# Kernel optimization log

Hardware: AMD Instinct MI355X
Metric: run time of the kernel (lower is better)

The kernel has to match this reference:

```python
import jax, jax.numpy as jnp
import numpy as np

HEAD_SIZE = 128
LAMBDA_INIT = 0.8
FILL = 1e-09  # the module fills masked positions with 1e-9 (not -inf); reproduce faithfully


def setup_inputs() -> dict:
    key = jax.random.key(0)
    ks = jax.random.split(key, 12)
    B, T, C = 8, 2048, 1024
    q = jax.random.normal(ks[0], (B, T, C), dtype=jnp.float32)
    k = jax.random.normal(ks[1], (B, T, C), dtype=jnp.float32)
    v = jax.random.normal(ks[2], (B, T, C), dtype=jnp.float32)
    pad_mask = jax.random.randint(ks[3], (B, T), 0, 2, dtype=jnp.int32)
    scale = 1.0 / np.sqrt(C)
    Wq = jax.random.normal(ks[4], (C, 2 * HEAD_SIZE), dtype=jnp.float32) * scale
    Wk = jax.random.normal(ks[5], (C, 2 * HEAD_SIZE), dtype=jnp.float32) * scale
    Wv = jax.random.normal(ks[6], (C, HEAD_SIZE), dtype=jnp.float32) * scale
    lq1 = jax.random.normal(ks[7], (HEAD_SIZE,), dtype=jnp.float32)
    lk1 = jax.random.normal(ks[8], (HEAD_SIZE,), dtype=jnp.float32)
    lq2 = jax.random.normal(ks[9], (HEAD_SIZE,), dtype=jnp.float32)
    lk2 = jax.random.normal(ks[10], (HEAD_SIZE,), dtype=jnp.float32)
    return {"q": q, "k": k, "v": v, "pad_mask": pad_mask,
            "Wq": Wq, "Wk": Wk, "Wv": Wv,
            "lq1": lq1, "lk1": lk1, "lq2": lq2, "lk2": lk2}


def reference(q, k, v, pad_mask, Wq, Wk, Wv, lq1, lk1, lq2, lk2):
    B, T_q, C = q.shape
    T_k = k.shape[1]
    Q = q @ Wq                      # [B, Tq, 2*hs]
    K = k @ Wk                      # [B, Tk, 2*hs]
    V = v @ Wv                      # [B, Tk, ho]
    Q1, Q2 = jnp.split(Q, 2, axis=-1)
    K1, K2 = jnp.split(K, 2, axis=-1)
    s1 = jnp.einsum("bqd,bkd->bqk", Q1, K1)
    s2 = jnp.einsum("bqd,bkd->bqk", Q2, K2)
    # causal mask: tril(ones, diagonal=1) == 0 -> fill (note diagonal=1, one lookahead)
    causal_fill = jnp.tril(jnp.ones((T_q, T_k), dtype=bool), 1) == False
    s1 = jnp.where(causal_fill[None], FILL, s1)
    s2 = jnp.where(causal_fill[None], FILL, s2)
    # pad mask broadcast over the KEY axis per query row (as in original)
    pad_fill = (pad_mask == 1)[:, :, None]  # [B, Tq, 1]
    s1 = jnp.where(pad_fill, FILL, s1)
    s2 = jnp.where(pad_fill, FILL, s2)
    scale = HEAD_SIZE ** (-0.5)
    lbd = jnp.exp(jnp.dot(lq1, lk1)) - jnp.exp(jnp.dot(lq2, lk2)) + LAMBDA_INIT
    attn = jax.nn.softmax(s1 * scale, axis=-1) - lbd * jax.nn.softmax(s2 * scale, axis=-1)
    return attn @ V                 # [B, Tq, ho]
```

## Files before the change

### kernel.cpp

```cpp
#include <hip/hip_runtime.h>
#include <math.h>


#define T_SEQ 2048
#define NB 8
#define CDIM 1024
#define HS 128

constexpr float SCALE = 0.08838834764831845f;

typedef float f32x4 __attribute__((ext_vector_type(4)));
typedef __bf16 bf16x8 __attribute__((ext_vector_type(8)));
typedef unsigned int u32;

#define MFMA16 __builtin_amdgcn_mfma_f32_16x16x32_bf16

__device__ __forceinline__ void gld16(const void* g, void* l) {
  __builtin_amdgcn_global_load_lds(
      (const __attribute__((address_space(1))) u32*)g,
      (__attribute__((address_space(3))) u32*)l, 16, 0, 0);
}

__device__ __forceinline__ bf16x8 cvt8(f32x4 lo, f32x4 hi) {
  bf16x8 r;
  r[0] = (__bf16)lo.x; r[1] = (__bf16)lo.y; r[2] = (__bf16)lo.z; r[3] = (__bf16)lo.w;
  r[4] = (__bf16)hi.x; r[5] = (__bf16)hi.y; r[6] = (__bf16)hi.z; r[7] = (__bf16)hi.w;
  return r;
}

__global__ __launch_bounds__(128) void lambda_kernel(
    const float* __restrict__ lq1, const float* __restrict__ lk1,
    const float* __restrict__ lq2, const float* __restrict__ lk2,
    float* __restrict__ lbd) {
  __shared__ float r1[128], r2[128];
  int t = threadIdx.x;
  r1[t] = lq1[t] * lk1[t];
  r2[t] = lq2[t] * lk2[t];
  __syncthreads();
  for (int s = 64; s > 0; s >>= 1) {
    if (t < s) { r1[t] += r1[t + s]; r2[t] += r2[t + s]; }
    __syncthreads();
  }
  if (t == 0) *lbd = expf(r1[0]) - expf(r2[0]) + 0.8f;
}

__global__ __launch_bounds__(256) void pack_w(
    const float* __restrict__ Wq, const float* __restrict__ Wk,
    const float* __restrict__ Wv, __bf16* __restrict__ Wp) {
  int nt = blockIdx.x;
  const float* W; int colbase, N;
  if (nt < 16)      { W = Wq; colbase = nt * 16;        N = 256; }
  else if (nt < 32) { W = Wk; colbase = (nt - 16) * 16; N = 256; }
  else              { W = Wv; colbase = (nt - 32) * 16; N = 128; }
  int tid = threadIdx.x;
#pragma unroll
  for (int i = 0; i < 8; ++i) {
    int u = tid + 256 * i;
    int ks = u >> 6, lane = u & 63;
    int l15 = lane & 15, quad = lane >> 4;
    bf16x8 pk;
#pragma unroll
    for (int j = 0; j < 8; ++j)
      pk[j] = (__bf16)W[(size_t)(ks * 32 + quad * 8 + j) * N + colbase + l15];
    *(bf16x8*)(Wp + ((size_t)(nt * 32 + ks) * 64 + lane) * 8) = pk;
  }
}

template<int NT, int NTG>
__device__ __forceinline__ void proj_body(
    const float* __restrict__ Ablk, const __bf16* __restrict__ Wp,
    __bf16* __restrict__ outp, __bf16* __restrict__ Vt,
    int rows0, char* smem) {
  float*  sA = (float*)smem;
  __bf16* sB = (__bf16*)(smem + 32768);
  const int tid = threadIdx.x;
  const int lane = tid & 63, wave = tid >> 6;
  const int l15 = lane & 15, quad = lane >> 4;
  const int arow = lane >> 3;
  const int ac16 = (lane & 7) ^ arow;

  f32x4 acc0[NT], acc1[NT];
#pragma unroll
  for (int j = 0; j < NT; ++j) {
    acc0[j] = (f32x4){0.f, 0.f, 0.f, 0.f};
    acc1[j] = (f32x4){0.f, 0.f, 0.f, 0.f};
  }

  auto stage_ks = [&](int ks, int buf) {
    const float* gA = Ablk + ks * 32;
    float* lA = sA + buf * 4096;
#pragma unroll
    for (int i = 0; i < 4; ++i) {
      int li = wave * 4 + i;
      gld16(gA + (size_t)(li * 8 + arow) * CDIM + ac16 * 4, lA + li * 256);
    }
    __bf16* lB = sB + buf * 8192;
#pragma unroll
    for (int i = 0; i < 4; ++i) {
      int ntl = wave * 4 + i;
      if (ntl < NT)
        gld16(Wp + ((size_t)((NTG + ntl) * 32 + ks) * 64 + lane) * 8,
              lB + ntl * 512);
    }
  };

  stage_ks(0, 0);
  for (int ks = 0; ks < 32; ++ks) {
    const int buf = ks & 1;
    __syncthreads();
    const float* lA = sA + buf * 4096;
    int r0 = wave * 32 + l15;
    f32x4 lo0 = *(const f32x4*)(lA + r0 * 32 + (((quad * 2)     ^ (l15 & 7)) * 4));
    f32x4 hi0 = *(const f32x4*)(lA + r0 * 32 + (((quad * 2 + 1) ^ (l15 & 7)) * 4));
    bf16x8 af0 = cvt8(lo0, hi0);
    int r1 = r0 + 16;
    f32x4 lo1 = *(const f32x4*)(lA + r1 * 32 + (((quad * 2)     ^ (l15 & 7)) * 4));
    f32x4 hi1 = *(const f32x4*)(lA + r1 * 32 + (((quad * 2 + 1) ^ (l15 & 7)) * 4));
    bf16x8 af1 = cvt8(lo1, hi1);
    if (ks < 31) stage_ks(ks + 1, buf ^ 1);
    const __bf16* lB = sB + buf * 8192;
#pragma unroll
    for (int nt = 0; nt < NT; ++nt) {
      bf16x8 bf = *(const bf16x8*)(lB + nt * 512 + lane * 8);
      acc0[nt] = MFMA16(af0, bf, acc0[nt], 0, 0, 0);
      acc1[nt] = MFMA16(af1, bf, acc1[nt], 0, 0, 0);
    }
  }

  __syncthreads();
  __bf16* tile = (__bf16*)smem;
  constexpr int N = NT * 16;
#pragma unroll
  for (int half = 0; half < (NT >> 3); ++half) {
#pragma unroll
    for (int ntl = 0; ntl < 8; ++ntl) {
      f32x4 a0 = acc0[half * 8 + ntl];
      f32x4 a1 = acc1[half * 8 + ntl];
#pragma unroll
      for (int r = 0; r < 4; ++r) {
        tile[(wave * 32 + quad * 4 + r) * 136 + ntl * 16 + l15] = (__bf16)a0[r];
        tile[(wave * 32 + 16 + quad * 4 + r) * 136 + ntl * 16 + l15] = (__bf16)a1[r];
      }
    }
    __syncthreads();
#pragma unroll
    for (int i = 0; i < 8; ++i) {
      int u = tid + 256 * i;
      int row = u >> 4, c8 = u & 15;
      bf16x8 val = *(const bf16x8*)(tile + row * 136 + c8 * 8);
      *(bf16x8*)(outp + (size_t)(rows0 + row) * N + half * 128 + c8 * 8) = val;
    }
    if constexpr (NT == 8) {
      int b = rows0 >> 11, t0 = rows0 & 2047;
#pragma unroll
      for (int i = 0; i < 8; ++i) {
        int u = tid + 256 * i;
        int tc = u & 15, c = u >> 4;
        bf16x8 pk;
#pragma unroll
        for (int j = 0; j < 8; ++j) pk[j] = tile[(tc * 8 + j) * 136 + c];
        *(bf16x8*)(Vt + ((size_t)(b * 128 + c)) * T_SEQ + t0 + tc * 8) = pk;
      }
    }
    __syncthreads();
  }
}

__global__ __launch_bounds__(256, 2) void proj_mfma(
    const float* __restrict__ qin, const float* __restrict__ kin,
    const float* __restrict__ vin, const __bf16* __restrict__ Wp,
    __bf16* __restrict__ Qo, __bf16* __restrict__ Ko,
    __bf16* __restrict__ Vo, __bf16* __restrict__ Vt) {
  __shared__ char smem[65536];
  const int blk = blockIdx.x;
  const int rows0 = (blk & 127) * 128;
  if (blk < 128)
    proj_body<16, 0>(qin + (size_t)rows0 * CDIM, Wp, Qo, nullptr, rows0, smem);
  else if (blk < 256)
    proj_body<16, 16>(kin + (size_t)rows0 * CDIM, Wp, Ko, nullptr, rows0, smem);
  else
    proj_body<8, 32>(vin + (size_t)rows0 * CDIM, Wp, Vo, Vt, rows0, smem);
}

__global__ __launch_bounds__(128) void vcsum_a(const __bf16* __restrict__ V,
                                               float* __restrict__ csum) {
  int blk = blockIdx.x; int b = blk >> 4, ch = blk & 15;
  int c = threadIdx.x;
  const __bf16* vp = V + ((size_t)b * T_SEQ + ch * 128) * HS + c;
  float s = 0.f;
#pragma unroll 4
  for (int t = 0; t < 128; ++t) s += (float)vp[(size_t)t * HS];
  csum[(size_t)blk * HS + c] = s;
}

__global__ __launch_bounds__(128) void vcsum_b(const __bf16* __restrict__ V,
                                               const float* __restrict__ csum,
                                               float* __restrict__ cum) {
  int blk = blockIdx.x; int b = blk >> 4, ch = blk & 15;
  int c = threadIdx.x;
  float run = 0.f;
  for (int j = 0; j < ch; ++j) run += csum[(size_t)(b * 16 + j) * HS + c];
  const __bf16* vp = V + ((size_t)b * T_SEQ + ch * 128) * HS + c;
  float* cp = cum + ((size_t)b * (T_SEQ + 1) + ch * 128) * HS + c;
  if (ch == 0) cp[0] = 0.f;
#pragma unroll 4
  for (int t = 0; t < 128; ++t) {
    run += (float)vp[(size_t)t * HS];
    cp[(size_t)(t + 1) * HS] = run;
  }
}

__global__ __launch_bounds__(512, 2) void attn_mfma(
    const __bf16* __restrict__ Q, const __bf16* __restrict__ K,
    const __bf16* __restrict__ Vt, const float* __restrict__ cum,
    const int* __restrict__ pad, const float* __restrict__ lbdp,
    float* __restrict__ out) {
  __shared__ __bf16 sQ[32 * 264];
  __shared__ __bf16 sP[2][2][32 * 136];
  __shared__ float zb[2][32][64];
  __shared__ float zfin[2][32];

  const int tid = threadIdx.x;
  const int lane = tid & 63, wave = tid >> 6;
  const int wm = wave >> 2, wk = wave & 3;
  const int l15 = lane & 15, quad = lane >> 4;

  const int p = blockIdx.x;
  const int b = p & 7, pr = p >> 3;
  const float lbd = *lbdp;
  const __bf16* Qb = Q + (size_t)b * T_SEQ * 256;
  const __bf16* Kb = K + (size_t)b * T_SEQ * 256;
  const __bf16* Vtb = Vt + (size_t)b * HS * T_SEQ;
  const float* cumb = cum + (size_t)b * (T_SEQ + 1) * HS;
  const float pc = (1.f - lbd) * (1.f / (float)T_SEQ);

  for (int ph = 0; ph < 2; ++ph) {
    const int ti = ph ? (63 - pr) : pr;
    const int q0 = ti * 32;

#pragma unroll
    for (int i = 0; i < 2; ++i) {
      int c = tid + 512 * i;
      int row = c >> 5, c16 = c & 31;
      *(f32x4*)(&sQ[row * 264 + c16 * 8]) =
          *(const f32x4*)(Qb + (size_t)(q0 + row) * 256 + c16 * 8);
    }
    __syncthreads();

    bf16x8 qf[2][4];
    {
      const int row = wm * 16 + l15;
#pragma unroll
      for (int pl = 0; pl < 2; ++pl)
#pragma unroll
        for (int s = 0; s < 4; ++s)
          qf[pl][s] = *(const bf16x8*)(&sQ[row * 264 + pl * 128 + s * 32 + quad * 8]);
    }

    f32x4 O[2][2];
#pragma unroll
    for (int i = 0; i < 2; ++i)
#pragma unroll
      for (int j = 0; j < 2; ++j) O[i][j] = (f32x4){0.f, 0.f, 0.f, 0.f};
    float z[2][4] = {};

    const int lastkey = q0 + 32;
    const int nkt = (min(lastkey, T_SEQ - 1) >> 7) + 1;

    for (int kt = 0; kt < nkt; ++kt) {
      const int k0 = kt << 7;
      const bool needmask = (k0 + 127 > q0 + 1);
      const int buf = kt & 1;

#pragma unroll
      for (int mat = 0; mat < 2; ++mat) {
        const __bf16* kp = Kb + (size_t)(k0 + wk * 32 + l15) * 256 + mat * 128 + quad * 8;
        bf16x8 ka0 = *(const bf16x8*)(kp);
        bf16x8 ka1 = *(const bf16x8*)(kp + 32);
        bf16x8 ka2 = *(const bf16x8*)(kp + 64);
        bf16x8 ka3 = *(const bf16x8*)(kp + 96);
        const __bf16* kq = kp + 16 * 256;
        bf16x8 kb0 = *(const bf16x8*)(kq);
        bf16x8 kb1 = *(const bf16x8*)(kq + 32);
        bf16x8 kb2 = *(const bf16x8*)(kq + 64);
        bf16x8 kb3 = *(const bf16x8*)(kq + 96);
        f32x4 S0 = (f32x4){0.f, 0.f, 0.f, 0.f}, S1 = S0;
        S0 = MFMA16(qf[mat][0], ka0, S0, 0, 0, 0);
        S0 = MFMA16(qf[mat][1], ka1, S0, 0, 0, 0);
        S0 = MFMA16(qf[mat][2], ka2, S0, 0, 0, 0);
        S0 = MFMA16(qf[mat][3], ka3, S0, 0, 0, 0);
        S1 = MFMA16(qf[mat][0], kb0, S1, 0, 0, 0);
        S1 = MFMA16(qf[mat][1], kb1, S1, 0, 0, 0);
        S1 = MFMA16(qf[mat][2], kb2, S1, 0, 0, 0);
        S1 = MFMA16(qf[mat][3], kb3, S1, 0, 0, 0);

        const int rowl = wm * 16 + quad * 4;
#pragma unroll
        for (int nt = 0; nt < 2; ++nt) {
          const int keyg = k0 + wk * 32 + nt * 16 + l15;
          const f32x4 Sv = nt ? S1 : S0;
#pragma unroll
          for (int r = 0; r < 4; ++r) {
            float pv;
            if (needmask) {
              int rowg = q0 + rowl + r;
              pv = (keyg <= rowg + 1) ? __expf(Sv[r] * SCALE) : 0.f;
            } else {
              pv = __expf(Sv[r] * SCALE);
            }
            z[mat][r] += pv;
            sP[buf][mat][(rowl + r) * 136 + wk * 32 + nt * 16 + l15] = (__bf16)pv;
          }
        }
      }
      __syncthreads();

#pragma unroll
      for (int ks = 0; ks < 4; ++ks) {
        bf16x8 pf0 = *(const bf16x8*)(&sP[buf][0][(wm * 16 + l15) * 136 + ks * 32 + quad * 8]);
        bf16x8 pf1 = *(const bf16x8*)(&sP[buf][1][(wm * 16 + l15) * 136 + ks * 32 + quad * 8]);
#pragma unroll
        for (int nt = 0; nt < 2; ++nt) {
          bf16x8 vf = *(const bf16x8*)(Vtb + (size_t)(wk * 32 + nt * 16 + l15) * T_SEQ +
                                       k0 + ks * 32 + quad * 8);
          O[0][nt] = MFMA16(pf0, vf, O[0][nt], 0, 0, 0);
          O[1][nt] = MFMA16(pf1, vf, O[1][nt], 0, 0, 0);
        }
      }
    }

#pragma unroll
    for (int mat = 0; mat < 2; ++mat)
#pragma unroll
      for (int r = 0; r < 4; ++r)
        zb[mat][wm * 16 + quad * 4 + r][wk * 16 + l15] = z[mat][r];
    __syncthreads();
    if (tid < 64) {
      int mat = tid >> 5, row = tid & 31;
      float s = 0.f;
#pragma unroll
      for (int j = 0; j < 64; ++j) s += zb[mat][row][(j + tid) & 63];
      zfin[mat][row] = s;
    }
    __syncthreads();

#pragma unroll
    for (int r = 0; r < 4; ++r) {
      const int rowl = wm * 16 + quad * 4 + r;
      const int rowg = q0 + rowl;
      const int nallow = min(rowg + 2, T_SEQ);
      const float nmask = (float)(T_SEQ - nallow);
      const float Z1 = zfin[0][rowl] + nmask;
      const float Z2 = zfin[1][rowl] + nmask;
      const float i1 = 1.f / Z1, i2 = lbd / Z2;
      const float tc = i1 - i2;
      const bool isp = (pad[b * T_SEQ + rowg] == 1);
#pragma unroll
      for (int nt = 0; nt < 2; ++nt) {
        const int col = wk * 32 + nt * 16 + l15;
        const float ct = cumb[(size_t)T_SEQ * HS + col];
        const float cn = cumb[(size_t)nallow * HS + col];
        float val = isp ? (pc * ct)
                        : (O[0][nt][r] * i1 - O[1][nt][r] * i2 + tc * (ct - cn));
        out[((size_t)b * T_SEQ + rowg) * HS + col] = val;
      }
    }
    __syncthreads();
  }
}

extern "C" void kernel_launch(void* const* d_in, const int* in_sizes, int n_in,
                              void* d_out, int out_size, void* d_ws, size_t ws_size,
                              hipStream_t stream) {
  (void)in_sizes; (void)n_in; (void)out_size; (void)ws_size;
  const float* q   = (const float*)d_in[0];
  const float* k   = (const float*)d_in[1];
  const float* v   = (const float*)d_in[2];
  const int*   pm  = (const int*)d_in[3];
  const float* Wq  = (const float*)d_in[4];
  const float* Wk  = (const float*)d_in[5];
  const float* Wv  = (const float*)d_in[6];
  const float* lq1 = (const float*)d_in[7];
  const float* lk1 = (const float*)d_in[8];
  const float* lq2 = (const float*)d_in[9];
  const float* lk2 = (const float*)d_in[10];
  float* out = (float*)d_out;
  char* ws = (char*)d_ws;

  float*  lbd  = (float*)ws;
  __bf16* Wp   = (__bf16*)(ws + 16);
  __bf16* Qp   = (__bf16*)(ws + 16 + 1310720);
  __bf16* Kp   = Qp + (size_t)NB * T_SEQ * 256;
  __bf16* Vp   = Kp + (size_t)NB * T_SEQ * 256;
  __bf16* Vt   = Vp + (size_t)NB * T_SEQ * HS;
  float*  cum  = (float*)(Vt + (size_t)NB * T_SEQ * HS);
  float*  csum = cum + (size_t)NB * (T_SEQ + 1) * HS;

  lambda_kernel<<<dim3(1), dim3(128), 0, stream>>>(lq1, lk1, lq2, lk2, lbd);
  pack_w<<<dim3(40), dim3(256), 0, stream>>>(Wq, Wk, Wv, Wp);
  proj_mfma<<<dim3(384), dim3(256), 0, stream>>>(q, k, v, Wp, Qp, Kp, Vp, Vt);
  vcsum_a<<<dim3(128), dim3(128), 0, stream>>>(Vp, csum);
  vcsum_b<<<dim3(128), dim3(128), 0, stream>>>(Vp, csum, cum);
  attn_mfma<<<dim3(256), dim3(512), 0, stream>>>(Qp, Kp, Vt, cum, pm, lbd, out);
}
```

Measured before the change: 377.0 us.

## Double attention key tile to 256 with 16 waves per block

The attention kernel grows from 8 to 16 waves per block and processes 256-key tiles instead of 128. Each wave now owns 32 keys for the score computation and one 16-column slice of the output, so there are half as many key-loop iterations and barriers per query tile. In exchange the block needs more LDS for P and the partial row sums, and __launch_bounds__(1024,4) limits registers per thread. The last key tile for each query block is also larger, so more masked work is wasted on the diagonal.

```diff
diff --git a/kernel.cpp b/kernel.cpp
--- a/kernel.cpp
+++ b/kernel.cpp
@@ -210,19 +210,19 @@
   }
 }
 
-__global__ __launch_bounds__(512, 2) void attn_mfma(
+__global__ __launch_bounds__(1024, 4) void attn_mfma(
     const __bf16* __restrict__ Q, const __bf16* __restrict__ K,
     const __bf16* __restrict__ Vt, const float* __restrict__ cum,
     const int* __restrict__ pad, const float* __restrict__ lbdp,
     float* __restrict__ out) {
   __shared__ __bf16 sQ[32 * 264];
-  __shared__ __bf16 sP[2][2][32 * 136];
-  __shared__ float zb[2][32][64];
+  __shared__ __bf16 sP[2][2][32 * 264];
+  __shared__ float zb[2][32][128];
   __shared__ float zfin[2][32];
 
   const int tid = threadIdx.x;
   const int lane = tid & 63, wave = tid >> 6;
-  const int wm = wave >> 2, wk = wave & 3;
+  const int wm = wave >> 3, wk = wave & 7;
   const int l15 = lane & 15, quad = lane >> 4;
 
   const int p = blockIdx.x;
@@ -238,10 +238,8 @@
     const int ti = ph ? (63 - pr) : pr;
     const int q0 = ti * 32;
 
-#pragma unroll
-    for (int i = 0; i < 2; ++i) {
-      int c = tid + 512 * i;
-      int row = c >> 5, c16 = c & 31;
+    {
+      int row = tid >> 5, c16 = tid & 31;
       *(f32x4*)(&sQ[row * 264 + c16 * 8]) =
           *(const f32x4*)(Qb + (size_t)(q0 + row) * 256 + c16 * 8);
     }
@@ -257,19 +255,17 @@
           qf[pl][s] = *(const bf16x8*)(&sQ[row * 264 + pl * 128 + s * 32 + quad * 8]);
     }
 
-    f32x4 O[2][2];
-#pragma unroll
-    for (int i = 0; i < 2; ++i)
-#pragma unroll
-      for (int j = 0; j < 2; ++j) O[i][j] = (f32x4){0.f, 0.f, 0.f, 0.f};
+    f32x4 O[2];
+    O[0] = (f32x4){0.f, 0.f, 0.f, 0.f};
+    O[1] = (f32x4){0.f, 0.f, 0.f, 0.f};
     float z[2][4] = {};
 
     const int lastkey = q0 + 32;
-    const int nkt = (min(lastkey, T_SEQ - 1) >> 7) + 1;
+    const int nkt = (min(lastkey, T_SEQ - 1) >> 8) + 1;
 
     for (int kt = 0; kt < nkt; ++kt) {
-      const int k0 = kt << 7;
-      const bool needmask = (k0 + 127 > q0 + 1);
+      const int k0 = kt << 8;
+      const bool needmask = (k0 + 255 > q0 + 1);
       const int buf = kt & 1;
 
 #pragma unroll
@@ -309,23 +305,20 @@
               pv = __expf(Sv[r] * SCALE);
             }
             z[mat][r] += pv;
-            sP[buf][mat][(rowl + r) * 136 + wk * 32 + nt * 16 + l15] = (__bf16)pv;
+            sP[buf][mat][(rowl + r) * 264 + wk * 32 + nt * 16 + l15] = (__bf16)pv;
           }
         }
       }
       __syncthreads();
 
 #pragma unroll
-      for (int ks = 0; ks < 4; ++ks) {
-        bf16x8 pf0 = *(const bf16x8*)(&sP[buf][0][(wm * 16 + l15) * 136 + ks * 32 + quad * 8]);
-        bf16x8 pf1 = *(const bf16x8*)(&sP[buf][1][(wm * 16 + l15) * 136 + ks * 32 + quad * 8]);
-#pragma unroll
-        for (int nt = 0; nt < 2; ++nt) {
-          bf16x8 vf = *(const bf16x8*)(Vtb + (size_t)(wk * 32 + nt * 16 + l15) * T_SEQ +
-                                       k0 + ks * 32 + quad * 8);
-          O[0][nt] = MFMA16(pf0, vf, O[0][nt], 0, 0, 0);
-          O[1][nt] = MFMA16(pf1, vf, O[1][nt], 0, 0, 0);
-        }
+      for (int ks = 0; ks < 8; ++ks) {
+        bf16x8 pf0 = *(const bf16x8*)(&sP[buf][0][(wm * 16 + l15) * 264 + ks * 32 + quad * 8]);
+        bf16x8 pf1 = *(const bf16x8*)(&sP[buf][1][(wm * 16 + l15) * 264 + ks * 32 + quad * 8]);
+        bf16x8 vf = *(const bf16x8*)(Vtb + (size_t)(wk * 16 + l15) * T_SEQ +
+                                     k0 + ks * 32 + quad * 8);
+        O[0] = MFMA16(pf0, vf, O[0], 0, 0, 0);
+        O[1] = MFMA16(pf1, vf, O[1], 0, 0, 0);
       }
     }
 
@@ -339,29 +332,28 @@
       int mat = tid >> 5, row = tid & 31;
       float s = 0.f;
 #pragma unroll
-      for (int j = 0; j < 64; ++j) s += zb[mat][row][(j + tid) & 63];
+      for (int j = 0; j < 128; ++j) s += zb[mat][row][(j + tid) & 127];
       zfin[mat][row] = s;
     }
     __syncthreads();
 
-#pragma unroll
-    for (int r = 0; r < 4; ++r) {
-      const int rowl = wm * 16 + quad * 4 + r;
-      const int rowg = q0 + rowl;
-      const int nallow = min(rowg + 2, T_SEQ);
-      const float nmask = (float)(T_SEQ - nallow);
-      const float Z1 = zfin[0][rowl] + nmask;
-      const float Z2 = zfin[1][rowl] + nmask;
-      const float i1 = 1.f / Z1, i2 = lbd / Z2;
-      const float tc = i1 - i2;
-      const bool isp = (pad[b * T_SEQ + rowg] == 1);
-#pragma unroll
-      for (int nt = 0; nt < 2; ++nt) {
-        const int col = wk * 32 + nt * 16 + l15;
-        const float ct = cumb[(size_t)T_SEQ * HS + col];
+    {
+      const int col = wk * 16 + l15;
+      const float ct = cumb[(size_t)T_SEQ * HS + col];
+#pragma unroll
+      for (int r = 0; r < 4; ++r) {
+        const int rowl = wm * 16 + quad * 4 + r;
+        const int rowg = q0 + rowl;
+        const int nallow = min(rowg + 2, T_SEQ);
+        const float nmask = (float)(T_SEQ - nallow);
+        const float Z1 = zfin[0][rowl] + nmask;
+        const float Z2 = zfin[1][rowl] + nmask;
+        const float i1 = 1.f / Z1, i2 = lbd / Z2;
+        const float tc = i1 - i2;
+        const bool isp = (pad[b * T_SEQ + rowg] == 1);
         const float cn = cumb[(size_t)nallow * HS + col];
         float val = isp ? (pc * ct)
-                        : (O[0][nt][r] * i1 - O[1][nt][r] * i2 + tc * (ct - cn));
+                        : (O[0][r] * i1 - O[1][r] * i2 + tc * (ct - cn));
         out[((size_t)b * T_SEQ + rowg) * HS + col] = val;
       }
     }
@@ -401,5 +393,5 @@
   proj_mfma<<<dim3(384), dim3(256), 0, stream>>>(q, k, v, Wp, Qp, Kp, Vp, Vt);
   vcsum_a<<<dim3(128), dim3(128), 0, stream>>>(Vp, csum);
   vcsum_b<<<dim3(128), dim3(128), 0, stream>>>(Vp, csum, cum);
-  attn_mfma<<<dim3(256), dim3(512), 0, stream>>>(Qp, Kp, Vt, cum, pm, lbd, out);
-}
+  attn_mfma<<<dim3(256), dim3(1024), 0, stream>>>(Qp, Kp, Vt, cum, pm, lbd, out);
+}
```

Result: slower. 399.6 us (+6.0%).
